# Optimization experiments

Hardware: AMD Instinct MI355X
Metric: run time of the kernel (lower is better)

The kernel has to match this reference:

```python
import jax, jax.numpy as jnp
import numpy as np

N_EMBD = 1024
NUM_HEADS = 16
HEAD_SIZE = 64


def setup_inputs() -> dict:
    key = jax.random.key(0)
    ks = jax.random.split(key, 6)
    B, T, C, hs = 2, 2048, N_EMBD, HEAD_SIZE
    s = 0.02
    return {
        "x": jax.random.normal(ks[0], (B, T, C), dtype=jnp.float32),
        "Wk": jax.random.normal(ks[1], (hs, C), dtype=jnp.float32) * s,  # torch Linear weight [out,in]
        "Wv": jax.random.normal(ks[2], (hs, C), dtype=jnp.float32) * s,
        "Wq": jax.random.normal(ks[3], (C, C), dtype=jnp.float32) * s,
        "Wp": jax.random.normal(ks[4], (C, C), dtype=jnp.float32) * s,
        "bp": jax.random.normal(ks[5], (C,), dtype=jnp.float32) * s,
    }


def reference(x, Wk, Wv, Wq, Wp, bp):
    B, T, C = x.shape
    H, hs = NUM_HEADS, HEAD_SIZE
    k = x @ Wk.T                      # [B,T,hs]
    v = x @ Wv.T                      # [B,T,hs]
    q = x @ Wq.T                      # [B,T,C]
    # Faithful to torch: raw view of [B,T,C] -> [B,H,T,hs] (row-major reshape, not transpose)
    q = q.reshape(B, H, T, hs)
    k = k.reshape(B, 1, T, hs)
    v = v.reshape(B, 1, T, hs)
    att = jnp.einsum("bhqd,bhkd->bhqk", q, jnp.broadcast_to(k, (B, 1, T, hs))) * (hs ** -0.5)
    mask = jnp.tril(jnp.ones((T, T), dtype=bool))[None, None]  # [1,1,T,T]
    att = jnp.where(mask, att, -jnp.inf)
    att = jax.nn.softmax(att, axis=-1)
    y = jnp.einsum("bhqk,bhkd->bhqd", att, jnp.broadcast_to(v, (B, 1, T, hs)))  # [B,H,T,hs]
    y = jnp.transpose(y, (0, 2, 1, 3)).reshape(B, T, C)
    return y @ Wp.T + bp
```

## Files before the change

### kernel.cpp

```cpp
#include <hip/hip_runtime.h>
#include <cstddef>
#include <cstdint>

#define B_N 2
#define T_N 2048
#define C_N 1024
#define H_N 16
#define HS_N 64
#define M_N (B_N * T_N)

typedef __attribute__((ext_vector_type(8))) short bf16x8;
typedef __attribute__((ext_vector_type(4))) float f32x4;
typedef __attribute__((ext_vector_type(4))) unsigned int u32x4;
typedef __attribute__((ext_vector_type(2))) unsigned int u32x2;

#define QSCALE 0.18033688011112042f

__device__ __forceinline__ ushort f2bf(float f) {
    union { float f; uint32_t u; } v; v.f = f;
    uint32_t r = v.u + 0x7fffu + ((v.u >> 16) & 1u);
    return (ushort)(r >> 16);
}
__device__ __forceinline__ unsigned pack2_trunc(float a, float b) {
    union { float f; uint32_t u; } x, y; x.f = a; y.f = b;
    return (x.u >> 16) | (y.u & 0xFFFF0000u);
}

#define GLL16(g, l)                                                         \
    __builtin_amdgcn_global_load_lds(                                       \
        (const __attribute__((address_space(1))) unsigned int*)(g),         \
        (__attribute__((address_space(3))) unsigned int*)(l), 16, 0, 0)

__global__ void cvt_all_kernel(const float* __restrict__ x,
                               const float* __restrict__ Wq,
                               const float* __restrict__ Wp,
                               const float* __restrict__ Wk,
                               const float* __restrict__ Wv,
                               ushort* __restrict__ xb,
                               ushort* __restrict__ Wqb,
                               ushort* __restrict__ Wpb,
                               ushort* __restrict__ Wkvb) {
    const int S0 = M_N * C_N / 4;
    const int S1 = S0 + C_N * C_N / 4;
    const int S2 = S1 + C_N * C_N / 4;
    const int S3 = S2 + HS_N * C_N / 4;
    const int S4 = S3 + HS_N * C_N / 4;
    const int stride = gridDim.x * blockDim.x;
    for (int i = blockIdx.x * blockDim.x + threadIdx.x; i < S4; i += stride) {
        const float* src; ushort* dst; int j; float sc = 1.f;
        if (i < S0)      { src = x;  dst = xb;   j = i; }
        else if (i < S1) { src = Wq; dst = Wqb;  j = i - S0; sc = QSCALE; }
        else if (i < S2) { src = Wp; dst = Wpb;  j = i - S1; }
        else if (i < S3) { src = Wk; dst = Wkvb; j = i - S2; }
        else             { src = Wv; dst = Wkvb + HS_N * C_N; j = i - S3; }
        const float4 f = ((const float4*)src)[j];
        ushort4 o;
        o.x = f2bf(f.x * sc); o.y = f2bf(f.y * sc);
        o.z = f2bf(f.z * sc); o.w = f2bf(f.w * sc);
        ((ushort4*)dst)[j] = o;
    }
}

template <int MODE>
__global__ __launch_bounds__(256, 2) void gemm_bf16(
    const ushort* __restrict__ A,
    const ushort* __restrict__ W,
    const float* __restrict__ bias,
    void* __restrict__ Cout,
    ushort* __restrict__ kb,
    ushort* __restrict__ vbt,
    int K)
{
    __shared__ __align__(16) ushort As0[64 * 64];
    __shared__ __align__(16) ushort Bs0[128 * 64];
    __shared__ __align__(16) ushort As1[64 * 64];
    __shared__ __align__(16) ushort Bs1[128 * 64];
    const int flat = blockIdx.x + (blockIdx.y << 6);
    const int m0 = (((flat & 7) << 3) | ((flat >> 3) & 7)) * 64;
    const int n0 = (flat >> 6) * 128;
    const int tid = threadIdx.x;
    const int wid = tid >> 6;
    const int lane = tid & 63;
    const int ln = lane & 15;
    const int quad = lane >> 4;
    const int wm = wid >> 1, wn = wid & 1;

    f32x4 acc[2][4];
    #pragma unroll
    for (int i = 0; i < 2; ++i)
        #pragma unroll
        for (int j = 0; j < 4; ++j)
            acc[i][j] = (f32x4){0.f, 0.f, 0.f, 0.f};

    const int srow = lane >> 3;
    const int schk = (lane & 7) ^ srow;

    auto stage = [&](ushort* Asb, ushort* Bsb, int k0) {
        #pragma unroll
        for (int t = 0; t < 2; ++t) {
            const int seg = wid * 2 + t;
            GLL16(A + (size_t)(m0 + seg * 8 + srow) * K + k0 + schk * 8,
                  Asb + seg * 512);
        }
        #pragma unroll
        for (int t = 0; t < 4; ++t) {
            const int seg = wid * 4 + t;
            GLL16(W + (size_t)(n0 + seg * 8 + srow) * K + k0 + schk * 8,
                  Bsb + seg * 512);
        }
    };

    auto compute = [&](const ushort* Asb, const ushort* Bsb) {
        #pragma unroll
        for (int hh = 0; hh < 2; ++hh) {
            bf16x8 af[2], bf[4];
            const int sw = ln & 7;
            #pragma unroll
            for (int i = 0; i < 2; ++i) {
                const int row = wm * 32 + i * 16 + ln;
                af[i] = *(const bf16x8*)&Asb[row * 64 + (((hh * 4 + quad) ^ sw) * 8)];
            }
            #pragma unroll
            for (int j = 0; j < 4; ++j) {
                const int row = wn * 64 + j * 16 + ln;
                bf[j] = *(const bf16x8*)&Bsb[row * 64 + (((hh * 4 + quad) ^ sw) * 8)];
            }
            #pragma unroll
            for (int i = 0; i < 2; ++i)
                #pragma unroll
                for (int j = 0; j < 4; ++j)
                    acc[i][j] = __builtin_amdgcn_mfma_f32_16x16x32_bf16(
                        af[i], bf[j], acc[i][j], 0, 0, 0);
        }
    };

    const int nk = K >> 6;
    stage(As0, Bs0, 0);
    __syncthreads();
    for (int kt = 0; kt < nk; kt += 2) {
        if (kt + 1 < nk) stage(As1, Bs1, (kt + 1) << 6);
        compute(As0, Bs0);
        __syncthreads();
        if (kt + 1 >= nk) break;
        if (kt + 2 < nk) stage(As0, Bs0, (kt + 2) << 6);
        compute(As1, Bs1);
        __syncthreads();
    }

    if (MODE == 1 && n0 >= C_N) {
        #pragma unroll
        for (int i = 0; i < 2; ++i) {
            const int row0 = m0 + wm * 32 + i * 16 + quad * 4;
            #pragma unroll
            for (int j = 0; j < 4; ++j) {
                const int c2 = wn * 64 + j * 16 + ln;
                if (c2 >= 64) {
                    const int d = c2 - 64;
                    const int b = row0 >> 11;
                    const int t0 = row0 & 2047;
                    const int flatv = ((((t0 >> 5) * 4 + (d >> 4)) * 4
                                       + ((t0 >> 3) & 3)) * 16 + (d & 15)) * 8
                                      + (t0 & 7);
                    ushort4 pk;
                    pk.x = f2bf(acc[i][j][0]); pk.y = f2bf(acc[i][j][1]);
                    pk.z = f2bf(acc[i][j][2]); pk.w = f2bf(acc[i][j][3]);
                    *(ushort4*)&vbt[(size_t)b * HS_N * T_N + flatv] = pk;
                } else {
                    #pragma unroll
                    for (int reg = 0; reg < 4; ++reg) {
                        const int key = row0 + reg;
                        kb[((((key >> 4) * 2 + (c2 >> 5)) * 4
                             + ((c2 >> 3) & 3)) * 16 + (key & 15)) * 8
                           + (c2 & 7)] = f2bf(acc[i][j][reg]);
                    }
                }
            }
        }
        return;
    }

    #pragma unroll
    for (int i = 0; i < 2; ++i) {
        #pragma unroll
        for (int j = 0; j < 4; ++j) {
            const int col = n0 + wn * 64 + j * 16 + ln;
            const float bv = (MODE == 0) ? bias[col] : 0.f;
            #pragma unroll
            for (int reg = 0; reg < 4; ++reg) {
                const int row = m0 + wm * 32 + i * 16 + quad * 4 + reg;
                const float v = acc[i][j][reg] + bv;
                if (MODE == 0)
                    ((float*)Cout)[(size_t)row * C_N + col] = v;
                else
                    ((ushort*)Cout)[(size_t)row * C_N + col] = f2bf(v);
            }
        }
    }
}

__global__ __launch_bounds__(256, 2) void attn_mfma_kernel(
    const ushort* __restrict__ qb,
    const ushort* __restrict__ kb,
    const ushort* __restrict__ vbt,
    ushort* __restrict__ yb)
{
    __shared__ __align__(16) float Ored[4 * 64 * 36];

    const int bh = blockIdx.x;
    const int b = bh >> 4, h = bh & 15;
    const int yy = blockIdx.y;
    const int qt = (yy < 8) ? 31 - yy : (yy < 16) ? yy - 8
                 : (yy < 24) ? 39 - yy : yy - 16;
    const int nkt = (qt >> 1) + 1;
    const int qmax = qt * 64 + 63;

    const int tid = threadIdx.x;
    const int w = tid >> 6;
    const int lane = tid & 63;
    const int ln = lane & 15;
    const int quad = lane >> 4;

    bf16x8 qf[4][2];
    {
        const ushort* qs_ = qb + (size_t)b * T_N * C_N
                          + (size_t)h * T_N * HS_N
                          + (size_t)(qt * 64) * HS_N;
        #pragma unroll
        for (int q4 = 0; q4 < 4; ++q4)
            #pragma unroll
            for (int kc = 0; kc < 2; ++kc)
                qf[q4][kc] = *(const bf16x8*)(qs_ + (q4 * 16 + ln) * HS_N
                                              + kc * 32 + quad * 8);
    }

    const ushort* vbb = vbt + (size_t)b * HS_N * T_N;

    f32x4 o[4][4];
    #pragma unroll
    for (int i = 0; i < 4; ++i)
        #pragma unroll
        for (int j = 0; j < 4; ++j)
            o[i][j] = (f32x4){0.f, 0.f, 0.f, 0.f};
    float lac[4] = {0.f, 0.f, 0.f, 0.f};

    for (int kt = 0; kt < nkt; ++kt) {
        const int k0 = kt * 128;
        const bool dg = (kt == nkt - 1);
        const int kw0 = k0 + w * 32;
        if (dg && kw0 > qmax) break;

        const int b16 = ((b * T_N + k0) >> 4) + w * 2;
        bf16x8 kf[2][2], vf[4];
        #pragma unroll
        for (int nt = 0; nt < 2; ++nt)
            #pragma unroll
            for (int kc = 0; kc < 2; ++kc)
                kf[nt][kc] = *(const bf16x8*)
                    &kb[((((b16 + nt) * 2 + kc) * 4 + quad) * 16 + ln) * 8];
        const int t32 = (k0 >> 5) + w;
        #pragma unroll
        for (int db = 0; db < 4; ++db)
            vf[db] = *(const bf16x8*)
                &vbb[(((t32 * 4 + db) * 4 + quad) * 16 + ln) * 8];

        f32x4 sc[2][4];
        #pragma unroll
        for (int nt = 0; nt < 2; ++nt)
            #pragma unroll
            for (int q4 = 0; q4 < 4; ++q4) {
                f32x4 s = (f32x4){0.f, 0.f, 0.f, 0.f};
                s = __builtin_amdgcn_mfma_f32_16x16x32_bf16(kf[nt][0], qf[q4][0], s, 0, 0, 0);
                s = __builtin_amdgcn_mfma_f32_16x16x32_bf16(kf[nt][1], qf[q4][1], s, 0, 0, 0);
                sc[nt][q4] = s;
            }

        unsigned pk[2][4][2];
        #pragma unroll
        for (int nt = 0; nt < 2; ++nt)
            #pragma unroll
            for (int q4 = 0; q4 < 4; ++q4) {
                f32x4 s = sc[nt][q4];
                if (dg) {
                    const int qg = qt * 64 + q4 * 16 + ln;
                    #pragma unroll
                    for (int reg = 0; reg < 4; ++reg) {
                        const int key = kw0 + nt * 16 + quad * 4 + reg;
                        if (key > qg) s[reg] = -1e30f;
                    }
                }
                const float p0 = __builtin_amdgcn_exp2f(s[0]);
                const float p1 = __builtin_amdgcn_exp2f(s[1]);
                const float p2 = __builtin_amdgcn_exp2f(s[2]);
                const float p3 = __builtin_amdgcn_exp2f(s[3]);
                lac[q4] += (p0 + p1) + (p2 + p3);
                pk[nt][q4][0] = pack2_trunc(p0, p1);
                pk[nt][q4][1] = pack2_trunc(p2, p3);
            }

        #pragma unroll
        for (int q4 = 0; q4 < 4; ++q4) {
            u32x2 ab0 = __builtin_amdgcn_permlane32_swap(pk[0][q4][0], pk[1][q4][0], false, false);
            u32x2 rs0 = __builtin_amdgcn_permlane16_swap(ab0[0], ab0[1], false, false);
            u32x2 ab1 = __builtin_amdgcn_permlane32_swap(pk[0][q4][1], pk[1][q4][1], false, false);
            u32x2 rs1 = __builtin_amdgcn_permlane16_swap(ab1[0], ab1[1], false, false);
            u32x4 pw;
            pw[0] = rs0[0]; pw[1] = rs1[0]; pw[2] = rs0[1]; pw[3] = rs1[1];
            const bf16x8 pf = __builtin_bit_cast(bf16x8, pw);
            #pragma unroll
            for (int db = 0; db < 4; ++db)
                o[db][q4] = __builtin_amdgcn_mfma_f32_16x16x32_bf16(
                    vf[db], pf, o[db][q4], 0, 0, 0);
        }
    }

    #pragma unroll
    for (int q4 = 0; q4 < 4; ++q4) {
        lac[q4] += __shfl_xor(lac[q4], 16);
        lac[q4] += __shfl_xor(lac[q4], 32);
    }

    const int qloc = 16 * w + (lane >> 2);
    float inv = 0.f;

    #pragma unroll
    for (int pass = 0; pass < 2; ++pass) {
        __syncthreads();
        #pragma unroll
        for (int db2 = 0; db2 < 2; ++db2)
            #pragma unroll
            for (int q4 = 0; q4 < 4; ++q4)
                *(f32x4*)&Ored[(w * 64 + q4 * 16 + ln) * 36 + db2 * 16 + quad * 4]
                    = o[pass * 2 + db2][q4];
        if (pass == 0 && quad == 0) {
            #pragma unroll
            for (int q4 = 0; q4 < 4; ++q4)
                Ored[(w * 64 + q4 * 16 + ln) * 36 + 32] = lac[q4];
        }
        __syncthreads();

        f32x4 a0 = (f32x4){0.f, 0.f, 0.f, 0.f};
        f32x4 a1 = (f32x4){0.f, 0.f, 0.f, 0.f};
        float ls = 0.f;
        #pragma unroll
        for (int v = 0; v < 4; ++v) {
            const int base = (v * 64 + qloc) * 36;
            a0 += *(const f32x4*)&Ored[base + (lane & 3) * 4];
            a1 += *(const f32x4*)&Ored[base + 16 + (lane & 3) * 4];
            if (pass == 0) ls += Ored[base + 32];
        }
        if (pass == 0) inv = 1.0f / ls;

        const int qg = qt * 64 + qloc;
        ushort* yrow = yb + ((size_t)b * T_N + qg) * C_N + h * HS_N
                       + pass * 32 + (lane & 3) * 4;
        ushort4 s0, s1;
        s0.x = f2bf(a0[0] * inv); s0.y = f2bf(a0[1] * inv);
        s0.z = f2bf(a0[2] * inv); s0.w = f2bf(a0[3] * inv);
        s1.x = f2bf(a1[0] * inv); s1.y = f2bf(a1[1] * inv);
        s1.z = f2bf(a1[2] * inv); s1.w = f2bf(a1[3] * inv);
        *(ushort4*)yrow = s0;
        *(ushort4*)(yrow + 16) = s1;
    }
}

extern "C" void kernel_launch(void* const* d_in, const int* in_sizes, int n_in,
                              void* d_out, int out_size, void* d_ws, size_t ws_size,
                              hipStream_t stream) {
    const float* x  = (const float*)d_in[0];
    const float* Wk = (const float*)d_in[1];
    const float* Wv = (const float*)d_in[2];
    const float* Wq = (const float*)d_in[3];
    const float* Wp = (const float*)d_in[4];
    const float* bp = (const float*)d_in[5];
    float* out = (float*)d_out;

    ushort* xb   = (ushort*)d_ws;
    ushort* qb   = xb   + (size_t)M_N * C_N;
    ushort* yb   = qb   + (size_t)M_N * C_N;
    ushort* kbw  = yb   + (size_t)M_N * C_N;
    ushort* vbt  = kbw  + (size_t)M_N * HS_N;
    ushort* Wqb  = vbt  + (size_t)B_N * HS_N * T_N;
    ushort* Wkvb = Wqb  + (size_t)C_N * C_N;
    ushort* Wpb  = Wkvb + (size_t)128 * C_N;

    cvt_all_kernel<<<1024, 256, 0, stream>>>(x, Wq, Wp, Wk, Wv,
                                             xb, Wqb, Wpb, Wkvb);

    gemm_bf16<1><<<dim3(M_N / 64, (C_N + 128) / 128), 256, 0, stream>>>(
        xb, Wqb, nullptr, qb, kbw, vbt, C_N);

    attn_mfma_kernel<<<dim3(B_N * H_N, 32), 256, 0, stream>>>(qb, kbw, vbt, yb);

    gemm_bf16<0><<<dim3(M_N / 64, C_N / 128), 256, 0, stream>>>(
        yb, Wpb, bp, out, nullptr, nullptr, C_N);
}
```

Baseline: 141.6 us.

## Double-buffer K/V tiles into per-wave LDS with async global-to-LDS loads

Replaces the direct global loads of K and V fragments inside the attention loop with async global-to-LDS copies (GLL16) into a per-wave double buffer. The next tile is prefetched while the current one is computed, with explicit vmcnt waits. The goal is to hide global memory latency behind the MFMA work. In exchange it grows shared memory to 64KB, which may reduce occupancy, and it relies on the GLL16 macro and vmcnt counts being correct.

```diff
diff --git a/kernel.cpp b/kernel.cpp
--- a/kernel.cpp
+++ b/kernel.cpp
@@ -204,7 +204,7 @@
     const ushort* __restrict__ vbt,
     ushort* __restrict__ yb)
 {
-    __shared__ __align__(16) float Ored[4 * 64 * 36];
+    __shared__ __align__(16) ushort smem[32768];
 
     const int bh = blockIdx.x;
     const int b = bh >> 4, h = bh & 15;
@@ -234,6 +234,24 @@
     }
 
     const ushort* vbb = vbt + (size_t)b * HS_N * T_N;
+    ushort* mybuf = smem + w * 8192;
+
+    auto stage = [&](int kt) {
+        const int k0 = kt * 128;
+        ushort* dst = mybuf + (kt & 1) * 4096;
+        const int b16 = ((b * T_N + k0) >> 4) + w * 2;
+        #pragma unroll
+        for (int nt = 0; nt < 2; ++nt)
+            #pragma unroll
+            for (int kc = 0; kc < 2; ++kc)
+                GLL16(kb + (size_t)((b16 + nt) * 2 + kc) * 512 + lane * 8,
+                      dst + (nt * 2 + kc) * 512);
+        const int t32 = (k0 >> 5) + w;
+        #pragma unroll
+        for (int db = 0; db < 4; ++db)
+            GLL16(vbb + (size_t)(t32 * 4 + db) * 512 + lane * 8,
+                  dst + (4 + db) * 512);
+    };
 
     f32x4 o[4][4];
     #pragma unroll
@@ -242,6 +260,8 @@
         for (int j = 0; j < 4; ++j)
             o[i][j] = (f32x4){0.f, 0.f, 0.f, 0.f};
     float lac[4] = {0.f, 0.f, 0.f, 0.f};
+
+    stage(0);
 
     for (int kt = 0; kt < nkt; ++kt) {
         const int k0 = kt * 128;
@@ -249,19 +269,26 @@
         const int kw0 = k0 + w * 32;
         if (dg && kw0 > qmax) break;
 
-        const int b16 = ((b * T_N + k0) >> 4) + w * 2;
+        if (kt + 1 < nkt) {
+            stage(kt + 1);
+            __builtin_amdgcn_sched_barrier(0);
+            asm volatile("s_waitcnt vmcnt(8)" ::: "memory");
+        } else {
+            __builtin_amdgcn_sched_barrier(0);
+            asm volatile("s_waitcnt vmcnt(0)" ::: "memory");
+        }
+        __builtin_amdgcn_sched_barrier(0);
+
+        const ushort* src = mybuf + (kt & 1) * 4096;
         bf16x8 kf[2][2], vf[4];
         #pragma unroll
         for (int nt = 0; nt < 2; ++nt)
             #pragma unroll
             for (int kc = 0; kc < 2; ++kc)
-                kf[nt][kc] = *(const bf16x8*)
-                    &kb[((((b16 + nt) * 2 + kc) * 4 + quad) * 16 + ln) * 8];
-        const int t32 = (k0 >> 5) + w;
+                kf[nt][kc] = *(const bf16x8*)&src[(nt * 2 + kc) * 512 + lane * 8];
         #pragma unroll
         for (int db = 0; db < 4; ++db)
-            vf[db] = *(const bf16x8*)
-                &vbb[(((t32 * 4 + db) * 4 + quad) * 16 + ln) * 8];
+            vf[db] = *(const bf16x8*)&src[(4 + db) * 512 + lane * 8];
 
         f32x4 sc[2][4];
         #pragma unroll
@@ -313,12 +340,15 @@
         }
     }
 
+    asm volatile("s_waitcnt vmcnt(0)" ::: "memory");
+
     #pragma unroll
     for (int q4 = 0; q4 < 4; ++q4) {
         lac[q4] += __shfl_xor(lac[q4], 16);
         lac[q4] += __shfl_xor(lac[q4], 32);
     }
 
+    float* Ored = (float*)smem;
     const int qloc = 16 * w + (lane >> 2);
     float inv = 0.f;
 
```

Result: slower. 144.8 us (+2.3%).
